# Performance work log

Hardware: AMD Instinct MI355X
Metric: run time of the kernel (lower is better)

## Reference

```python
import jax, jax.numpy as jnp
import numpy as np

B, T, D, H = 2, 2048, 1024, 16
DH = D // H


def setup_inputs() -> dict:
    key = jax.random.key(0)
    ks = jax.random.split(key, 5)
    scale = 1.0 / np.sqrt(D)
    return {
        "x": jax.random.normal(ks[0], (B, T, D), dtype=jnp.float32),
        "Wq": jax.random.normal(ks[1], (D, D), dtype=jnp.float32) * scale,
        "Wk": jax.random.normal(ks[2], (D, D), dtype=jnp.float32) * scale,
        "Wv": jax.random.normal(ks[3], (D, D), dtype=jnp.float32) * scale,
        "Wo": jax.random.normal(ks[4], (D, D), dtype=jnp.float32) * scale,
    }


def _split(y):
    # (B,T,D) -> (B,H,T,DH)
    b, t, _ = y.shape
    return y.reshape(b, t, H, DH).transpose(0, 2, 1, 3)


def reference(x, Wq, Wk, Wv, Wo):
    q = _split(x @ Wq)
    k = _split(x @ Wk)
    v = _split(x @ Wv)
    scores = jnp.einsum("bhqd,bhkd->bhqk", q, k) / jnp.sqrt(jnp.float32(DH))
    t = x.shape[1]
    # additive causal mask: -1e9 above the diagonal (matches band_part logic)
    causal = jnp.tril(jnp.ones((t, t), dtype=jnp.float32))
    scores = scores + (1.0 - causal) * -1e9
    attn = jax.nn.softmax(scores, axis=-1)
    out = jnp.einsum("bhqk,bhkd->bhqd", attn, v)  # (B,H,T,DH)
    out = out.transpose(0, 2, 1, 3).reshape(x.shape[0], t, D)
    return out @ Wo
```

## Files before the change

### kernel.cpp

```cpp
#include <hip/hip_runtime.h>

#define BB 2
#define TT 2048
#define DD 1024
#define HH 16
#define DHD 64
#define MM (BB*TT)

typedef __attribute__((ext_vector_type(8))) short short8;
typedef __attribute__((ext_vector_type(4))) float float4v;
typedef unsigned short u16;

__device__ inline float bf2f(u16 u) {
    union { unsigned int i; float f; } v;
    v.i = ((unsigned int)u) << 16;
    return v.f;
}
__device__ inline u16 f2bf(float f) {
    union { float f; unsigned int i; } v;
    v.f = f;
    unsigned int x = v.i;
    unsigned int r = (x + 0x7fffu + ((x >> 16) & 1u)) >> 16;
    return (u16)r;
}

__device__ inline void gl_lds16(const u16* g, u16* l) {
    __builtin_amdgcn_global_load_lds(
        (const __attribute__((address_space(1))) unsigned int*)g,
        (__attribute__((address_space(3))) unsigned int*)l, 16, 0, 0);
}

__global__ __launch_bounds__(256) void prep_k(const float* __restrict__ x,
                                              const float* __restrict__ Wq,
                                              const float* __restrict__ Wk,
                                              const float* __restrict__ Wv,
                                              const float* __restrict__ Wo,
                                              u16* __restrict__ xb,
                                              u16* __restrict__ WT) {
    int tid = threadIdx.x;
    if (blockIdx.z == 4) {
        int bid = blockIdx.y * 32 + blockIdx.x;
#pragma unroll
        for (int k = 0; k < 4; k++) {
            int i = bid * 1024 + k * 256 + tid;
            float4v v = ((const float4v*)x)[i];
            ushort4 o;
            o.x = f2bf(v[0]); o.y = f2bf(v[1]); o.z = f2bf(v[2]); o.w = f2bf(v[3]);
            ((ushort4*)xb)[i] = o;
        }
        return;
    }
    __shared__ u16 t[32][33];
    int wsel = blockIdx.z;
    const float* W = (wsel == 0) ? Wq : (wsel == 1) ? Wk : (wsel == 2) ? Wv : Wo;
    u16* o = WT + (size_t)wsel * DD * DD;
    int k0 = blockIdx.y * 32, n0 = blockIdx.x * 32;
    int tx = tid & 31, ty = tid >> 5;
#pragma unroll
    for (int i = 0; i < 4; i++) {
        int k = ty + i * 8;
        t[k][tx] = f2bf(W[(size_t)(k0 + k) * DD + n0 + tx]);
    }
    __syncthreads();
#pragma unroll
    for (int i = 0; i < 4; i++) {
        int n = ty + i * 8;
        o[(size_t)(n0 + n) * DD + k0 + tx] = t[tx][n];
    }
}

template <int MODE, int TM, int TN, int BK>
__global__ __launch_bounds__(256) void gemm_k(const u16* __restrict__ A,
                                              const u16* __restrict__ WT0,
                                              void* __restrict__ outp) {
    const int K = DD;
    const int MT = TM / 32, NT = TN / 32;
    const int NS = (TM + TN) * (BK / 8) / 256;
    const int CPR = BK / 8;

    int z = blockIdx.z;
    const u16* WT = WT0 + (size_t)z * DD * DD;
    int n0 = blockIdx.x * TN, m0 = blockIdx.y * TM;

    __shared__ u16 S[(TM + TN) * BK];

    int tid = threadIdx.x;
    int lane = tid & 63, w = tid >> 6;
    int wm = (w >> 1) * (TM / 2), wn = (w & 1) * (TN / 2);
    int quad = lane >> 4, l16 = lane & 15;

    const u16* gp[NS];
    u16* lp[NS];
#pragma unroll
    for (int j = 0; j < NS; j++) {
        int cid = tid + j * 256;
        int r = cid / CPR, c = cid % CPR;
        lp[j] = S + (size_t)cid * 8;
        gp[j] = (r < TM ? A + (size_t)(m0 + r) * K
                        : WT + (size_t)(n0 + r - TM) * K) + ((c ^ (r & 7)) * 8);
    }
    int swz = l16 & 7;

    float4v acc[MT][NT];
#pragma unroll
    for (int i = 0; i < MT; i++)
#pragma unroll
        for (int j = 0; j < NT; j++) acc[i][j] = (float4v)(0.0f);

    const int NK = K / BK;
#pragma unroll 1
    for (int ki = 0; ki < NK; ki++) {
        __syncthreads();
#pragma unroll
        for (int j = 0; j < NS; j++)
            gl_lds16(gp[j] + ki * BK, lp[j]);
        __syncthreads();

#pragma unroll
        for (int ks = 0; ks < BK / 32; ks++) {
            int cq = ((ks * 4 + quad) ^ swz) * 8;
            short8 a[MT], b[NT];
#pragma unroll
            for (int mt = 0; mt < MT; mt++)
                a[mt] = *(const short8*)&S[(wm + mt * 16 + l16) * BK + cq];
#pragma unroll
            for (int nt = 0; nt < NT; nt++)
                b[nt] = *(const short8*)&S[(TM + wn + nt * 16 + l16) * BK + cq];
#pragma unroll
            for (int mt = 0; mt < MT; mt++)
#pragma unroll
                for (int nt = 0; nt < NT; nt++)
                    acc[mt][nt] = __builtin_amdgcn_mfma_f32_16x16x32_bf16(
                        a[mt], b[nt], acc[mt][nt], 0, 0, 0);
        }
    }

#pragma unroll
    for (int mt = 0; mt < MT; mt++) {
#pragma unroll
        for (int nt = 0; nt < NT; nt++) {
#pragma unroll
            for (int r = 0; r < 4; r++) {
                int m = m0 + wm + mt * 16 + quad * 4 + r;
                int n = n0 + wn + nt * 16 + l16;
                float v = acc[mt][nt][r];
                if constexpr (MODE == 0) {
                    int bb = m >> 11, t = m & 2047;
                    int h = n >> 6, dh = n & 63;
                    size_t idx;
                    if (z == 2)
                        idx = (((size_t)2 * BB * HH + bb * HH + h) * DHD + dh) * TT + t;
                    else
                        idx = (((size_t)z * BB * HH + bb * HH + h) * TT + t) * DHD + dh;
                    ((u16*)outp)[idx] = f2bf(v);
                } else {
                    ((float*)outp)[(size_t)m * DD + n] = v;
                }
            }
        }
    }
}

__global__ __launch_bounds__(512) void attn_k(const u16* __restrict__ QKV,
                                              u16* __restrict__ AO) {
    const u16* Q  = QKV;
    const u16* Kp = QKV + (size_t)MM * DD;
    const u16* Vp = QKV + (size_t)2 * MM * DD;
    int bh = blockIdx.x;
    int qt = 31 - blockIdx.y;
    size_t hoff = (size_t)bh * TT * DHD;

    __shared__ u16 Ks[2][2][64 * 64];
    __shared__ u16 VTs[2][2][64 * 64];
    __shared__ u16 Ps[8][16 * 64];

    int tid = threadIdx.x;
    int lane = tid & 63, wv = tid >> 6;
    int g = wv >> 2, w4 = wv & 3;
    int quad = lane >> 4, l16 = lane & 15;
    int cxs = l16 & 7;

    int sr = tid >> 3, sc = tid & 7;
    int sl = sr * 64 + ((sc ^ (sr & 7)) * 8);
    const u16* gK = Kp + hoff + (size_t)sr * DHD + sc * 8;
    const u16* gV = Vp + hoff + (size_t)sr * TT + sc * 8;

    u16* Qstage = &Ps[0][0];

    const float qscale = 0.125f * 1.4426950408889634f;
    int q0 = qt * 64;
    {
        short8 v = *(const short8*)(Q + hoff + (size_t)(q0 + sr) * DHD + sc * 8);
        short8 sv;
#pragma unroll
        for (int e = 0; e < 8; e++) sv[e] = (short)f2bf(bf2f((u16)v[e]) * qscale);
        *(short8*)&Qstage[sl] = sv;
    }

    short8 prK[2], prV[2];
    prK[0] = *(const short8*)gK;
    prK[1] = *(const short8*)(gK + (size_t)64 * DHD);
    prV[0] = *(const short8*)gV;
    prV[1] = *(const short8*)(gV + 64);

    __syncthreads();
    int fr = w4 * 16 + l16;
    short8 aq0 = *(const short8*)&Qstage[fr * 64 + ((quad ^ cxs) * 8)];
    short8 aq1 = *(const short8*)&Qstage[fr * 64 + (((4 + quad) ^ cxs) * 8)];

    int NR = (qt >> 1) + 1;

    float4v o[4];
#pragma unroll
    for (int i = 0; i < 4; i++) o[i] = (float4v)(0.0f);
    float lr = 0.0f;

#pragma unroll 1
    for (int jt = 0; jt < NR; jt++) {
        int db = jt & 1;
#pragma unroll
        for (int tt = 0; tt < 2; tt++) {
            *(short8*)&Ks[db][tt][sl]  = prK[tt];
            *(short8*)&VTs[db][tt][sl] = prV[tt];
        }
        __syncthreads();

        if (jt + 1 < NR) {
            size_t nj = (size_t)(jt + 1) * 128;
            prK[0] = *(const short8*)(gK + nj * DHD);
            prK[1] = *(const short8*)(gK + (nj + 64) * DHD);
            prV[0] = *(const short8*)(gV + nj);
            prV[1] = *(const short8*)(gV + nj + 64);
        }

        int tj = 2 * jt + g;
        if (tj <= qt) {
            float4v s[4];
#pragma unroll
            for (int ct = 0; ct < 4; ct++) {
                int kr = (ct * 16 + l16) * 64;
                short8 ak0 = *(const short8*)&Ks[db][g][kr + ((quad ^ cxs) * 8)];
                short8 ak1 = *(const short8*)&Ks[db][g][kr + (((4 + quad) ^ cxs) * 8)];
                float4v sv = (float4v)(0.0f);
                sv = __builtin_amdgcn_mfma_f32_16x16x32_bf16(ak0, aq0, sv, 0, 0, 0);
                sv = __builtin_amdgcn_mfma_f32_16x16x32_bf16(ak1, aq1, sv, 0, 0, 0);
                s[ct] = sv;
            }

            if (tj == qt) {
                int ql = w4 * 16 + l16;
#pragma unroll
                for (int ct = 0; ct < 4; ct++)
#pragma unroll
                    for (int r = 0; r < 4; r++) {
                        int kvl = ct * 16 + quad * 4 + r;
                        if (kvl > ql) s[ct][r] = -30000.0f;
                    }
            }

#pragma unroll
            for (int ct = 0; ct < 4; ct++) {
                float p0 = __builtin_amdgcn_exp2f(s[ct][0]);
                float p1 = __builtin_amdgcn_exp2f(s[ct][1]);
                float p2 = __builtin_amdgcn_exp2f(s[ct][2]);
                float p3 = __builtin_amdgcn_exp2f(s[ct][3]);
                lr += (p0 + p1) + (p2 + p3);
                union { float f; unsigned u; } c0, c1, c2, c3;
                c0.f = p0; c1.f = p1; c2.f = p2; c3.f = p3;
                ushort4 pw;
                pw.x = (u16)(c0.u >> 16);
                pw.y = (u16)(c1.u >> 16);
                pw.z = (u16)(c2.u >> 16);
                pw.w = (u16)(c3.u >> 16);
                int chnk = (ct * 2 + (quad >> 1)) ^ cxs;
                *(ushort4*)&Ps[wv][l16 * 64 + chnk * 8 + (quad & 1) * 4] = pw;
            }

            short8 ap0 = *(const short8*)&Ps[wv][l16 * 64 + ((quad ^ cxs) * 8)];
            short8 ap1 = *(const short8*)&Ps[wv][l16 * 64 + (((4 + quad) ^ cxs) * 8)];
#pragma unroll
            for (int ct = 0; ct < 4; ct++) {
                int vr = (ct * 16 + l16) * 64;
                short8 bv0 = *(const short8*)&VTs[db][g][vr + ((quad ^ cxs) * 8)];
                short8 bv1 = *(const short8*)&VTs[db][g][vr + (((4 + quad) ^ cxs) * 8)];
                o[ct] = __builtin_amdgcn_mfma_f32_16x16x32_bf16(ap0, bv0, o[ct], 0, 0, 0);
                o[ct] = __builtin_amdgcn_mfma_f32_16x16x32_bf16(ap1, bv1, o[ct], 0, 0, 0);
            }
        }
    }

    __syncthreads();
    float* Of = (float*)&Ks[0][0][0];
    float* Lf = (float*)&VTs[0][0][0];
    if (g == 1) {
#pragma unroll
        for (int ct = 0; ct < 4; ct++)
#pragma unroll
            for (int r = 0; r < 4; r++)
                Of[(((w4 * 4 + ct) * 4 + r) * 64) + lane] = o[ct][r];
        Lf[w4 * 64 + lane] = lr;
    }
    __syncthreads();
    if (g == 0) {
#pragma unroll
        for (int ct = 0; ct < 4; ct++)
#pragma unroll
            for (int r = 0; r < 4; r++)
                o[ct][r] += Of[(((w4 * 4 + ct) * 4 + r) * 64) + lane];
        lr += Lf[w4 * 64 + lane];

        float rs = lr;
        rs += __shfl_xor(rs, 16);
        rs += __shfl_xor(rs, 32);
        int gbase = lane & 48;
        float rinv[4];
#pragma unroll
        for (int r = 0; r < 4; r++)
            rinv[r] = 1.0f / __shfl(rs, gbase + quad * 4 + r);

        int b = bh >> 4, h = bh & 15;
#pragma unroll
        for (int ct = 0; ct < 4; ct++) {
#pragma unroll
            for (int r = 0; r < 4; r++) {
                int q = q0 + w4 * 16 + quad * 4 + r;
                int d = h * 64 + ct * 16 + l16;
                AO[(size_t)(b * TT + q) * DD + d] = f2bf(o[ct][r] * rinv[r]);
            }
        }
    }
}

extern "C" void kernel_launch(void* const* d_in, const int* in_sizes, int n_in,
                              void* d_out, int out_size, void* d_ws, size_t ws_size,
                              hipStream_t stream) {
    const float* x  = (const float*)d_in[0];
    const float* Wq = (const float*)d_in[1];
    const float* Wk = (const float*)d_in[2];
    const float* Wv = (const float*)d_in[3];
    const float* Wo = (const float*)d_in[4];

    u16* xb  = (u16*)d_ws;
    u16* WT  = xb + (size_t)MM * DD;
    u16* QKV = WT + (size_t)4 * DD * DD;
    u16* AO  = QKV + (size_t)3 * MM * DD;
    float* out = (float*)d_out;

    prep_k<<<dim3(32, 32, 5), 256, 0, stream>>>(x, Wq, Wk, Wv, Wo, xb, WT);
    gemm_k<0, 128, 128, 64><<<dim3(DD / 128, MM / 128, 3), 256, 0, stream>>>(xb, WT, QKV);
    attn_k<<<dim3(32, 32), 512, 0, stream>>>(QKV, AO);
    gemm_k<1, 64, 128, 64><<<dim3(DD / 128, MM / 64, 1), 256, 0, stream>>>(AO, WT + (size_t)3 * DD * DD, out);
}
```

Baseline: 167.0 us.

## Process 128 query rows per attention block instead of splitting KV across wave groups

Each attention block now covers 128 query rows, with all 8 waves owning distinct query rows and walking both 64-key sub-tiles, instead of two wave groups splitting the KV range for 64 queries. Each K/V tile loaded into shared memory is therefore reused by twice as many queries, and the cross-group LDS reduction at the end goes away. Q is loaded straight into registers without LDS staging, and the block order is interleaved to balance causal work; launch bounds request 4 blocks per CU. The trade-off is half as many blocks and longer per-block loops, which may reduce parallelism and load balance.

```diff
diff --git a/kernel.cpp b/kernel.cpp
--- a/kernel.cpp
+++ b/kernel.cpp
@@ -161,13 +161,14 @@
     }
 }
 
-__global__ __launch_bounds__(512) void attn_k(const u16* __restrict__ QKV,
-                                              u16* __restrict__ AO) {
+__global__ __launch_bounds__(512, 4) void attn_k(const u16* __restrict__ QKV,
+                                                 u16* __restrict__ AO) {
     const u16* Q  = QKV;
     const u16* Kp = QKV + (size_t)MM * DD;
     const u16* Vp = QKV + (size_t)2 * MM * DD;
     int bh = blockIdx.x;
-    int qt = 31 - blockIdx.y;
+    int by = blockIdx.y;
+    int qt = (by < 8) ? (15 - by) : (by - 8);
     size_t hoff = (size_t)bh * TT * DHD;
 
     __shared__ u16 Ks[2][2][64 * 64];
@@ -176,7 +177,6 @@
 
     int tid = threadIdx.x;
     int lane = tid & 63, wv = tid >> 6;
-    int g = wv >> 2, w4 = wv & 3;
     int quad = lane >> 4, l16 = lane & 15;
     int cxs = l16 & 7;
 
@@ -185,16 +185,19 @@
     const u16* gK = Kp + hoff + (size_t)sr * DHD + sc * 8;
     const u16* gV = Vp + hoff + (size_t)sr * TT + sc * 8;
 
-    u16* Qstage = &Ps[0][0];
-
     const float qscale = 0.125f * 1.4426950408889634f;
-    int q0 = qt * 64;
+    int q0 = qt * 128;
+    int ql = wv * 16 + l16;
+    short8 aq0, aq1;
     {
-        short8 v = *(const short8*)(Q + hoff + (size_t)(q0 + sr) * DHD + sc * 8);
-        short8 sv;
-#pragma unroll
-        for (int e = 0; e < 8; e++) sv[e] = (short)f2bf(bf2f((u16)v[e]) * qscale);
-        *(short8*)&Qstage[sl] = sv;
+        const u16* gq = Q + hoff + (size_t)(q0 + ql) * DHD;
+        short8 v0 = *(const short8*)(gq + quad * 8);
+        short8 v1 = *(const short8*)(gq + 32 + quad * 8);
+#pragma unroll
+        for (int e = 0; e < 8; e++) {
+            aq0[e] = (short)f2bf(bf2f((u16)v0[e]) * qscale);
+            aq1[e] = (short)f2bf(bf2f((u16)v1[e]) * qscale);
+        }
     }
 
     short8 prK[2], prV[2];
@@ -203,12 +206,7 @@
     prV[0] = *(const short8*)gV;
     prV[1] = *(const short8*)(gV + 64);
 
-    __syncthreads();
-    int fr = w4 * 16 + l16;
-    short8 aq0 = *(const short8*)&Qstage[fr * 64 + ((quad ^ cxs) * 8)];
-    short8 aq1 = *(const short8*)&Qstage[fr * 64 + (((4 + quad) ^ cxs) * 8)];
-
-    int NR = (qt >> 1) + 1;
+    const int NR = qt + 1;
 
     float4v o[4];
 #pragma unroll
@@ -233,28 +231,30 @@
             prV[1] = *(const short8*)(gV + nj + 64);
         }
 
-        int tj = 2 * jt + g;
-        if (tj <= qt) {
+#pragma unroll
+        for (int tt = 0; tt < 2; tt++) {
+            int lim = ql - tt * 64;
+            if (jt == qt && lim < 0) continue;
+
             float4v s[4];
 #pragma unroll
             for (int ct = 0; ct < 4; ct++) {
                 int kr = (ct * 16 + l16) * 64;
-                short8 ak0 = *(const short8*)&Ks[db][g][kr + ((quad ^ cxs) * 8)];
-                short8 ak1 = *(const short8*)&Ks[db][g][kr + (((4 + quad) ^ cxs) * 8)];
+                short8 ak0 = *(const short8*)&Ks[db][tt][kr + ((quad ^ cxs) * 8)];
+                short8 ak1 = *(const short8*)&Ks[db][tt][kr + (((4 + quad) ^ cxs) * 8)];
                 float4v sv = (float4v)(0.0f);
                 sv = __builtin_amdgcn_mfma_f32_16x16x32_bf16(ak0, aq0, sv, 0, 0, 0);
                 sv = __builtin_amdgcn_mfma_f32_16x16x32_bf16(ak1, aq1, sv, 0, 0, 0);
                 s[ct] = sv;
             }
 
-            if (tj == qt) {
-                int ql = w4 * 16 + l16;
+            if (jt == qt) {
 #pragma unroll
                 for (int ct = 0; ct < 4; ct++)
 #pragma unroll
                     for (int r = 0; r < 4; r++) {
                         int kvl = ct * 16 + quad * 4 + r;
-                        if (kvl > ql) s[ct][r] = -30000.0f;
+                        if (kvl > lim) s[ct][r] = -30000.0f;
                     }
             }
 
@@ -281,52 +281,31 @@
 #pragma unroll
             for (int ct = 0; ct < 4; ct++) {
                 int vr = (ct * 16 + l16) * 64;
-                short8 bv0 = *(const short8*)&VTs[db][g][vr + ((quad ^ cxs) * 8)];
-                short8 bv1 = *(const short8*)&VTs[db][g][vr + (((4 + quad) ^ cxs) * 8)];
+                short8 bv0 = *(const short8*)&VTs[db][tt][vr + ((quad ^ cxs) * 8)];
+                short8 bv1 = *(const short8*)&VTs[db][tt][vr + (((4 + quad) ^ cxs) * 8)];
                 o[ct] = __builtin_amdgcn_mfma_f32_16x16x32_bf16(ap0, bv0, o[ct], 0, 0, 0);
                 o[ct] = __builtin_amdgcn_mfma_f32_16x16x32_bf16(ap1, bv1, o[ct], 0, 0, 0);
             }
         }
     }
 
-    __syncthreads();
-    float* Of = (float*)&Ks[0][0][0];
-    float* Lf = (float*)&VTs[0][0][0];
-    if (g == 1) {
-#pragma unroll
-        for (int ct = 0; ct < 4; ct++)
-#pragma unroll
-            for (int r = 0; r < 4; r++)
-                Of[(((w4 * 4 + ct) * 4 + r) * 64) + lane] = o[ct][r];
-        Lf[w4 * 64 + lane] = lr;
-    }
-    __syncthreads();
-    if (g == 0) {
-#pragma unroll
-        for (int ct = 0; ct < 4; ct++)
-#pragma unroll
-            for (int r = 0; r < 4; r++)
-                o[ct][r] += Of[(((w4 * 4 + ct) * 4 + r) * 64) + lane];
-        lr += Lf[w4 * 64 + lane];
-
-        float rs = lr;
-        rs += __shfl_xor(rs, 16);
-        rs += __shfl_xor(rs, 32);
-        int gbase = lane & 48;
-        float rinv[4];
-#pragma unroll
-        for (int r = 0; r < 4; r++)
-            rinv[r] = 1.0f / __shfl(rs, gbase + quad * 4 + r);
-
-        int b = bh >> 4, h = bh & 15;
-#pragma unroll
-        for (int ct = 0; ct < 4; ct++) {
-#pragma unroll
-            for (int r = 0; r < 4; r++) {
-                int q = q0 + w4 * 16 + quad * 4 + r;
-                int d = h * 64 + ct * 16 + l16;
-                AO[(size_t)(b * TT + q) * DD + d] = f2bf(o[ct][r] * rinv[r]);
-            }
+    float rs = lr;
+    rs += __shfl_xor(rs, 16);
+    rs += __shfl_xor(rs, 32);
+    int gbase = lane & 48;
+    float rinv[4];
+#pragma unroll
+    for (int r = 0; r < 4; r++)
+        rinv[r] = 1.0f / __shfl(rs, gbase + quad * 4 + r);
+
+    int b = bh >> 4, h = bh & 15;
+#pragma unroll
+    for (int ct = 0; ct < 4; ct++) {
+#pragma unroll
+        for (int r = 0; r < 4; r++) {
+            int q = q0 + wv * 16 + quad * 4 + r;
+            int d = h * 64 + ct * 16 + l16;
+            AO[(size_t)(b * TT + q) * DD + d] = f2bf(o[ct][r] * rinv[r]);
         }
     }
 }
@@ -348,6 +327,6 @@
 
     prep_k<<<dim3(32, 32, 5), 256, 0, stream>>>(x, Wq, Wk, Wv, Wo, xb, WT);
     gemm_k<0, 128, 128, 64><<<dim3(DD / 128, MM / 128, 3), 256, 0, stream>>>(xb, WT, QKV);
-    attn_k<<<dim3(32, 32), 512, 0, stream>>>(QKV, AO);
+    attn_k<<<dim3(32, 16), 512, 0, stream>>>(QKV, AO);
     gemm_k<1, 64, 128, 64><<<dim3(DD / 128, MM / 64, 1), 256, 0, stream>>>(AO, WT + (size_t)3 * DD * DD, out);
 }
```

Result: no change. 168.8 us (+1.1%).

## Add 256x256 double-buffered MFMA GEMM kernel for QKV projection

Applied to the files above, without the earlier changes.

Replaces the templated 128x128 QKV projection GEMM with a dedicated 512-thread kernel that computes 256x256 output tiles per block. It uses double-buffered LDS filled by direct global-to-LDS loads, an XOR-swizzled layout to avoid bank conflicts, and 16x16x32 bf16 MFMAs with 8x4 accumulator tiles per wave. This raises arithmetic intensity and overlaps the next K-tile's loads with the current tile's compute. The grid shrinks to 192 blocks, which may underfill the GPU's CUs, and the larger accumulator set raises register pressure. The weight-transpose store in prep is also vectorized to ushort4 writes.

```diff
diff --git a/kernel.cpp b/kernel.cpp
--- a/kernel.cpp
+++ b/kernel.cpp
@@ -62,10 +62,102 @@
         t[k][tx] = f2bf(W[(size_t)(k0 + k) * DD + n0 + tx]);
     }
     __syncthreads();
-#pragma unroll
-    for (int i = 0; i < 4; i++) {
-        int n = ty + i * 8;
-        o[(size_t)(n0 + n) * DD + k0 + tx] = t[tx][n];
+    int n = tid >> 3, kc = tid & 7;
+    ushort4 w4v;
+    w4v.x = t[kc * 4 + 0][n];
+    w4v.y = t[kc * 4 + 1][n];
+    w4v.z = t[kc * 4 + 2][n];
+    w4v.w = t[kc * 4 + 3][n];
+    *(ushort4*)&o[(size_t)(n0 + n) * DD + k0 + kc * 4] = w4v;
+}
+
+__global__ __launch_bounds__(512, 2) void gemmq_k(const u16* __restrict__ A,
+                                                  const u16* __restrict__ WT0,
+                                                  u16* __restrict__ outp) {
+    const int K = DD;
+    int z = blockIdx.z;
+    const u16* WT = WT0 + (size_t)z * DD * DD;
+    int n0 = blockIdx.x * 256, m0 = blockIdx.y * 256;
+
+    __shared__ u16 S[2 * 512 * 64];
+
+    int tid = threadIdx.x;
+    int lane = tid & 63, w = tid >> 6;
+    int wm = (w >> 2) * 128, wn = (w & 3) * 64;
+    int quad = lane >> 4, l16 = lane & 15;
+    int swz = l16 & 7;
+
+    const u16* gp[8];
+    u16* lp[8];
+#pragma unroll
+    for (int j = 0; j < 8; j++) {
+        int cid = tid + j * 512;
+        int r = cid >> 3, c = cid & 7;
+        lp[j] = S + (size_t)cid * 8;
+        gp[j] = (r < 256 ? A + (size_t)(m0 + r) * K
+                         : WT + (size_t)(n0 + r - 256) * K) + ((c ^ (r & 7)) * 8);
+    }
+
+    float4v acc[8][4];
+#pragma unroll
+    for (int i = 0; i < 8; i++)
+#pragma unroll
+        for (int j = 0; j < 4; j++) acc[i][j] = (float4v)(0.0f);
+
+#pragma unroll
+    for (int j = 0; j < 8; j++) gl_lds16(gp[j], lp[j]);
+    __syncthreads();
+
+    const int NK = K / 64;
+#pragma unroll 1
+    for (int kt = 0; kt < NK; kt++) {
+        if (kt + 1 < NK) {
+            int so = ((kt + 1) & 1) * 32768;
+#pragma unroll
+            for (int j = 0; j < 8; j++)
+                gl_lds16(gp[j] + (kt + 1) * 64, lp[j] + so);
+        }
+
+        const u16* Sb = S + (kt & 1) * 32768;
+#pragma unroll
+        for (int ks = 0; ks < 2; ks++) {
+            int cq = ((ks * 4 + quad) ^ swz) * 8;
+            short8 a[8], b[4];
+#pragma unroll
+            for (int mt = 0; mt < 8; mt++)
+                a[mt] = *(const short8*)&Sb[(wm + mt * 16 + l16) * 64 + cq];
+#pragma unroll
+            for (int nt = 0; nt < 4; nt++)
+                b[nt] = *(const short8*)&Sb[(256 + wn + nt * 16 + l16) * 64 + cq];
+#pragma unroll
+            for (int mt = 0; mt < 8; mt++)
+#pragma unroll
+                for (int nt = 0; nt < 4; nt++)
+                    acc[mt][nt] = __builtin_amdgcn_mfma_f32_16x16x32_bf16(
+                        a[mt], b[nt], acc[mt][nt], 0, 0, 0);
+        }
+        __syncthreads();
+    }
+
+#pragma unroll
+    for (int mt = 0; mt < 8; mt++) {
+#pragma unroll
+        for (int nt = 0; nt < 4; nt++) {
+#pragma unroll
+            for (int r = 0; r < 4; r++) {
+                int m = m0 + wm + mt * 16 + quad * 4 + r;
+                int n = n0 + wn + nt * 16 + l16;
+                float v = acc[mt][nt][r];
+                int bb = m >> 11, t = m & 2047;
+                int h = n >> 6, dh = n & 63;
+                size_t idx;
+                if (z == 2)
+                    idx = (((size_t)2 * BB * HH + bb * HH + h) * DHD + dh) * TT + t;
+                else
+                    idx = (((size_t)z * BB * HH + bb * HH + h) * TT + t) * DHD + dh;
+                outp[idx] = f2bf(v);
+            }
+        }
     }
 }
 
@@ -347,7 +439,7 @@
     float* out = (float*)d_out;
 
     prep_k<<<dim3(32, 32, 5), 256, 0, stream>>>(x, Wq, Wk, Wv, Wo, xb, WT);
-    gemm_k<0, 128, 128, 64><<<dim3(DD / 128, MM / 128, 3), 256, 0, stream>>>(xb, WT, QKV);
+    gemmq_k<<<dim3(DD / 256, MM / 256, 3), 512, 0, stream>>>(xb, WT, QKV);
     attn_k<<<dim3(32, 32), 512, 0, stream>>>(QKV, AO);
     gemm_k<1, 64, 128, 64><<<dim3(DD / 128, MM / 64, 1), 256, 0, stream>>>(AO, WT + (size_t)3 * DD * DD, out);
 }
```

Measured after the change: 188.6 us. 13.0% more time.

## Triple-buffer GEMM LDS loads with vmcnt waits and vectorize weight transpose stores

Applied to the files above, without the earlier changes.

Replaces the single-buffered GEMM loop, which had two full barriers per K step, with a three-slot LDS ring at BK=32. Loads are prefetched two tiles ahead and the wait uses explicit s_waitcnt vmcnt, so global-to-LDS traffic overlaps the MFMA work. The weight-transpose kernel now writes 8-byte vectors instead of scalar 2-byte stores. The smaller K tile means more loop iterations and barriers, and the hand-written vmcnt counts depend on how the compiler orders memory operations.

```diff
diff --git a/kernel.cpp b/kernel.cpp
--- a/kernel.cpp
+++ b/kernel.cpp
@@ -28,6 +28,14 @@
     __builtin_amdgcn_global_load_lds(
         (const __attribute__((address_space(1))) unsigned int*)g,
         (__attribute__((address_space(3))) unsigned int*)l, 16, 0, 0);
+}
+
+template <int N> __device__ inline void wait_vmcnt() {
+    if constexpr (N == 0) asm volatile("s_waitcnt vmcnt(0)" ::: "memory");
+    else if constexpr (N == 3) asm volatile("s_waitcnt vmcnt(3)" ::: "memory");
+    else if constexpr (N == 4) asm volatile("s_waitcnt vmcnt(4)" ::: "memory");
+    else if constexpr (N == 6) asm volatile("s_waitcnt vmcnt(6)" ::: "memory");
+    else if constexpr (N == 8) asm volatile("s_waitcnt vmcnt(8)" ::: "memory");
 }
 
 __global__ __launch_bounds__(256) void prep_k(const float* __restrict__ x,
@@ -62,44 +70,49 @@
         t[k][tx] = f2bf(W[(size_t)(k0 + k) * DD + n0 + tx]);
     }
     __syncthreads();
-#pragma unroll
-    for (int i = 0; i < 4; i++) {
-        int n = ty + i * 8;
-        o[(size_t)(n0 + n) * DD + k0 + tx] = t[tx][n];
-    }
-}
-
-template <int MODE, int TM, int TN, int BK>
-__global__ __launch_bounds__(256) void gemm_k(const u16* __restrict__ A,
-                                              const u16* __restrict__ WT0,
-                                              void* __restrict__ outp) {
+    int n = tid >> 3, kc = tid & 7;
+    ushort4 w4v;
+    w4v.x = t[kc * 4 + 0][n];
+    w4v.y = t[kc * 4 + 1][n];
+    w4v.z = t[kc * 4 + 2][n];
+    w4v.w = t[kc * 4 + 3][n];
+    *(ushort4*)&o[(size_t)(n0 + n) * DD + k0 + kc * 4] = w4v;
+}
+
+template <int MODE, int TM, int TN>
+__global__ __launch_bounds__(256) void gemm_k2(const u16* __restrict__ A,
+                                               const u16* __restrict__ WT0,
+                                               void* __restrict__ outp) {
+    const int BK = 32;
     const int K = DD;
+    const int NK = K / BK;
     const int MT = TM / 32, NT = TN / 32;
-    const int NS = (TM + TN) * (BK / 8) / 256;
-    const int CPR = BK / 8;
+    const int ROWS = TM + TN;
+    const int CH = ROWS / 64;
+    const int SLOT = ROWS * BK;
 
     int z = blockIdx.z;
     const u16* WT = WT0 + (size_t)z * DD * DD;
     int n0 = blockIdx.x * TN, m0 = blockIdx.y * TM;
 
-    __shared__ u16 S[(TM + TN) * BK];
+    __shared__ u16 S[3 * SLOT];
 
     int tid = threadIdx.x;
     int lane = tid & 63, w = tid >> 6;
     int wm = (w >> 1) * (TM / 2), wn = (w & 1) * (TN / 2);
     int quad = lane >> 4, l16 = lane & 15;
-
-    const u16* gp[NS];
-    u16* lp[NS];
-#pragma unroll
-    for (int j = 0; j < NS; j++) {
+    int swz = l16 & 3;
+
+    const u16* gp[CH];
+    u16* lp[CH];
+#pragma unroll
+    for (int j = 0; j < CH; j++) {
         int cid = tid + j * 256;
-        int r = cid / CPR, c = cid % CPR;
+        int r = cid >> 2, c = cid & 3;
         lp[j] = S + (size_t)cid * 8;
         gp[j] = (r < TM ? A + (size_t)(m0 + r) * K
-                        : WT + (size_t)(n0 + r - TM) * K) + ((c ^ (r & 7)) * 8);
-    }
-    int swz = l16 & 7;
+                        : WT + (size_t)(n0 + r - TM) * K) + ((c ^ (r & 3)) * 8);
+    }
 
     float4v acc[MT][NT];
 #pragma unroll
@@ -107,31 +120,43 @@
 #pragma unroll
         for (int j = 0; j < NT; j++) acc[i][j] = (float4v)(0.0f);
 
-    const int NK = K / BK;
+#pragma unroll
+    for (int j = 0; j < CH; j++) gl_lds16(gp[j], lp[j]);
+#pragma unroll
+    for (int j = 0; j < CH; j++) gl_lds16(gp[j] + BK, lp[j] + SLOT);
+    wait_vmcnt<CH>();
+    __builtin_amdgcn_s_barrier();
+    __builtin_amdgcn_sched_barrier(0);
+
 #pragma unroll 1
-    for (int ki = 0; ki < NK; ki++) {
-        __syncthreads();
-#pragma unroll
-        for (int j = 0; j < NS; j++)
-            gl_lds16(gp[j] + ki * BK, lp[j]);
-        __syncthreads();
-
-#pragma unroll
-        for (int ks = 0; ks < BK / 32; ks++) {
-            int cq = ((ks * 4 + quad) ^ swz) * 8;
-            short8 a[MT], b[NT];
-#pragma unroll
-            for (int mt = 0; mt < MT; mt++)
-                a[mt] = *(const short8*)&S[(wm + mt * 16 + l16) * BK + cq];
+    for (int kt = 0; kt < NK; kt++) {
+        if (kt + 2 < NK) {
+            int so = ((kt + 2) % 3) * SLOT;
+            int go = (kt + 2) * BK;
+#pragma unroll
+            for (int j = 0; j < CH; j++) gl_lds16(gp[j] + go, lp[j] + so);
+        }
+
+        const u16* Sb = S + (kt % 3) * SLOT;
+        int cq = (quad ^ swz) * 8;
+        short8 a[MT], b[NT];
+#pragma unroll
+        for (int mt = 0; mt < MT; mt++)
+            a[mt] = *(const short8*)&Sb[(wm + mt * 16 + l16) * BK + cq];
+#pragma unroll
+        for (int nt = 0; nt < NT; nt++)
+            b[nt] = *(const short8*)&Sb[(TM + wn + nt * 16 + l16) * BK + cq];
+#pragma unroll
+        for (int mt = 0; mt < MT; mt++)
 #pragma unroll
             for (int nt = 0; nt < NT; nt++)
-                b[nt] = *(const short8*)&S[(TM + wn + nt * 16 + l16) * BK + cq];
-#pragma unroll
-            for (int mt = 0; mt < MT; mt++)
-#pragma unroll
-                for (int nt = 0; nt < NT; nt++)
-                    acc[mt][nt] = __builtin_amdgcn_mfma_f32_16x16x32_bf16(
-                        a[mt], b[nt], acc[mt][nt], 0, 0, 0);
+                acc[mt][nt] = __builtin_amdgcn_mfma_f32_16x16x32_bf16(
+                    a[mt], b[nt], acc[mt][nt], 0, 0, 0);
+
+        if (kt + 1 < NK) {
+            if (kt + 2 < NK) wait_vmcnt<CH>(); else wait_vmcnt<0>();
+            __builtin_amdgcn_s_barrier();
+            __builtin_amdgcn_sched_barrier(0);
         }
     }
 
@@ -347,7 +372,7 @@
     float* out = (float*)d_out;
 
     prep_k<<<dim3(32, 32, 5), 256, 0, stream>>>(x, Wq, Wk, Wv, Wo, xb, WT);
-    gemm_k<0, 128, 128, 64><<<dim3(DD / 128, MM / 128, 3), 256, 0, stream>>>(xb, WT, QKV);
+    gemm_k2<0, 128, 128><<<dim3(DD / 128, MM / 128, 3), 256, 0, stream>>>(xb, WT, QKV);
     attn_k<<<dim3(32, 32), 512, 0, stream>>>(QKV, AO);
-    gemm_k<1, 64, 128, 64><<<dim3(DD / 128, MM / 64, 1), 256, 0, stream>>>(AO, WT + (size_t)3 * DD * DD, out);
-}
+    gemm_k2<1, 64, 128><<<dim3(DD / 128, MM / 64, 1), 256, 0, stream>>>(AO, WT + (size_t)3 * DD * DD, out);
+}
```

New measurement: 176.2 us. 5.5% more time.
